# Performance work log

Measured on AMD Instinct MI355X. Metric: run time of the kernel, lower is better.

Reference implementation:

```python
import jax, jax.numpy as jnp
import numpy as np
from jax import lax


def _conv1x1(x, w, b=None):
    # x: [N,C,H,W], w: [O,C]
    y = jnp.einsum('nchw,oc->nohw', x, w)
    if b is not None:
        y = y + b[None, :, None, None]
    return y


def _bn(x, g, b, rm, rv):
    # eval-mode BatchNorm2d, eps=1e-5 (torch default)
    inv = g / jnp.sqrt(rv + 1e-5)
    return x * inv[None, :, None, None] + (b - rm * inv)[None, :, None, None]


def setup_inputs() -> dict:
    key = jax.random.key(0)
    ks = jax.random.split(key, 32)
    N, C1, C2, H, W = 16, 256, 256, 64, 64
    mid = C2 // 16  # local_att reduction=16
    f32 = jnp.float32
    def nrm(k, shp, s=0.05):
        return s * jax.random.normal(k, shp, f32)
    return dict(
        x1=jax.random.normal(ks[0], (N, C1, H, W), f32),
        x2=jax.random.normal(ks[1], (N, C2, H, W), f32),
        conv1_w=nrm(ks[2], (C2, C1)), conv1_b=nrm(ks[3], (C2,)),
        conv2_w=nrm(ks[4], (C2, C2)), conv2_b=nrm(ks[5], (C2,)),
        conv3_w=nrm(ks[6], (C2, C2)), conv3_b=nrm(ks[7], (C2,)),
        conv4_w=nrm(ks[8], (C2, C2)), conv4_b=nrm(ks[9], (C2,)),
        conv4g_w=nrm(ks[10], (1, C2)), conv4g_b=nrm(ks[11], (1,)),
        bn_g=1.0 + nrm(ks[12], (C2,)), bn_b=nrm(ks[13], (C2,)),
        bn_rm=nrm(ks[14], (C2,)), bn_rv=1.0 + 0.1 * jax.random.uniform(ks[15], (C2,), f32),
        gamma=jax.random.normal(ks[16], (C2, 1, 1), f32), beta=jnp.zeros((C2, 1, 1), f32),
        gate_w=nrm(ks[17], (C2, C2)), gate_b=nrm(ks[18], (C2,)),
        dw_w=nrm(ks[19], (C2, 1, 3, 3)), dw_b=nrm(ks[20], (C2,)),
        interact_w=nrm(ks[21], (C2 // 4, C2 // 4)), interact_b=0.5 + nrm(ks[22], (C2 // 4,)),
        ca_w=nrm(ks[23], (1, 1, 5)),  # channel_att conv1d kernel, k=5 for C=256
        la1_w=nrm(ks[24], (mid, C2)),
        la_bn_g=1.0 + nrm(ks[25], (mid,)), la_bn_b=nrm(ks[26], (mid,)),
        la_bn_rm=nrm(ks[27], (mid,)), la_bn_rv=1.0 + 0.1 * jax.random.uniform(ks[28], (mid,), f32),
        fh_w=nrm(ks[29], (C2, mid)), fw_w=nrm(ks[30], (C2, mid)),
    )


def reference(x1, x2, conv1_w, conv1_b, conv2_w, conv2_b, conv3_w, conv3_b,
              conv4_w, conv4_b, conv4g_w, conv4g_b, bn_g, bn_b, bn_rm, bn_rv,
              gamma, beta, gate_w, gate_b, dw_w, dw_b, interact_w, interact_b,
              ca_w, la1_w, la_bn_g, la_bn_b, la_bn_rm, la_bn_rv, fh_w, fw_w):
    N, _, H, W = x1.shape
    C = conv1_w.shape[0]
    g1 = _conv1x1(x1, conv1_w, conv1_b)
    w1 = jax.nn.sigmoid(_bn(g1, bn_g, bn_b, bn_rm, bn_rv))
    g2 = _conv1x1(x2, conv2_w, conv2_b)
    w2 = jax.nn.sigmoid(_bn(g2, bn_g, bn_b, bn_rm, bn_rv))
    XG = g1 + g2

    # channel_att: GAP -> conv1d(k=5) across channels -> sigmoid gate
    y = XG.mean((2, 3))[:, None, :]  # [N,1,C]
    y = lax.conv_general_dilated(y, ca_w, (1,), [(2, 2)],
                                 dimension_numbers=('NCH', 'OIH', 'NCH'))
    temp = XG * jax.nn.sigmoid(y[:, 0, :])[:, :, None, None]

    # spatial sigmoid gate then 4-way group interact + softmax reweight
    Xs = jax.nn.sigmoid(_conv1x1(XG, conv4g_w, conv4g_b)) * XG
    C4 = C // 4
    Xr = Xs.reshape(N, 4, C4, H, W)
    o1 = jnp.einsum('ngchw,oc->ngohw', Xr, interact_w) + interact_b[None, None, :, None, None]
    xmap = o1.reshape(N, 4, 1, C4 * H * W)
    xav = xmap / xmap.mean(-1, keepdims=True)
    soft = jax.nn.softmax(xav, axis=2)  # softmax over size-1 dim -> ones (faithful)
    out = (soft.reshape(N, 4, C4, H, W) * Xr).reshape(N, C, H, W)

    # per-group (16) normalization using X_GOBAL stats (std unbiased, ddof=1)
    GN = 16
    xs = XG.reshape(N, GN, -1)
    mu = xs.mean(-1, keepdims=True)
    sd = jnp.std(xs, axis=-1, keepdims=True, ddof=1)
    x_gui = ((out.reshape(N, GN, -1) - mu) / (sd + 1e-10)).reshape(N, C, H, W)
    x_gui = x_gui * gamma[None] + beta[None]

    # threshold masks vs global-avg sigmoid reweights
    rw = jax.nn.sigmoid(XG.mean((2, 3), keepdims=True))  # [N,C,1,1]
    up1 = rw >= w1
    up2 = rw >= w2
    zero = jnp.zeros((), XG.dtype)
    x_up = jnp.where(up1, XG, zero) + jnp.where(up2, XG, zero)
    x_low = jnp.where(~up1, XG, zero) + jnp.where(~up2, XG, zero)

    # low branch: dwconv3x3 -> 1x1 -> channel-softmax gate
    dw = lax.conv_general_dilated(x_low, dw_w, (1, 1), [(1, 1), (1, 1)],
                                  dimension_numbers=('NCHW', 'OIHW', 'NCHW'),
                                  feature_group_count=C) + dw_b[None, :, None, None]
    x11 = _conv1x1(dw, conv3_w, conv3_b)
    gate = jax.nn.softmax(jax.nn.relu(x_low.mean((2, 3)) @ gate_w.T + gate_b), axis=1)
    xL = x11 * gate[:, :, None, None] + _conv1x1(x_up, conv4_w, conv4_b) + x_gui + temp

    # local_att (coordinate attention)
    xh = jnp.swapaxes(xL.mean(3, keepdims=True), 2, 3)  # [N,C,1,H]
    xw = xL.mean(2, keepdims=True)                       # [N,C,1,W]
    yc = jax.nn.relu(_bn(_conv1x1(jnp.concatenate([xh, xw], 3), la1_w),
                         la_bn_g, la_bn_b, la_bn_rm, la_bn_rv))
    sh = jax.nn.sigmoid(_conv1x1(jnp.swapaxes(yc[..., :H], 2, 3), fh_w))  # [N,C,H,1]
    sw = jax.nn.sigmoid(_conv1x1(yc[..., H:], fw_w))                      # [N,C,1,W]
    return xL * sh * sw
```

## Files before the change

kernel.cpp:

```cpp
#include <hip/hip_runtime.h>
#include <cstddef>
#include <cstdint>

constexpr int NN = 16, CC = 256, HH = 64, WW = 64, HW = 64 * 64;
constexpr size_t FSZ = (size_t)NN * CC * HW;

typedef short bf16x8 __attribute__((ext_vector_type(8)));
typedef float f32x4 __attribute__((ext_vector_type(4)));

__device__ __forceinline__ float sigmoidf_(float x) { return 1.f / (1.f + expf(-x)); }

__device__ __forceinline__ unsigned short bf16_rne(float f) {
    uint32_t u = __builtin_bit_cast(uint32_t, f);
    u += 0x7FFFu + ((u >> 16) & 1u);
    return (unsigned short)(u >> 16);
}
__device__ __forceinline__ float bf16_tof(unsigned short h) {
    uint32_t u = ((uint32_t)h) << 16;
    return __builtin_bit_cast(float, u);
}


__global__ __launch_bounds__(256) void wsplit_kernel(
    const float* __restrict__ w1, const float* __restrict__ w2,
    const float* __restrict__ w3, const float* __restrict__ w4,
    unsigned short* __restrict__ w1h, unsigned short* __restrict__ w1m, unsigned short* __restrict__ w1l,
    unsigned short* __restrict__ w2h, unsigned short* __restrict__ w2m, unsigned short* __restrict__ w2l,
    unsigned short* __restrict__ w4h, unsigned short* __restrict__ w4l,
    unsigned short* __restrict__ w3b,
    float* __restrict__ zstat, float* __restrict__ zspix) {
    const int i = blockIdx.x * 256 + threadIdx.x;
    const int o = i >> 8, c = i & 255;
    const size_t fo = ((size_t)((o >> 4) * 8 + (c >> 5))) * 512 +
                      (size_t)(((c & 31) >> 3) * 128 + (o & 15) * 8 + (c & 7));
    {
        float x = w1[i];
        unsigned short h = bf16_rne(x); float r = x - bf16_tof(h);
        unsigned short m = bf16_rne(r); float r2 = r - bf16_tof(m);
        w1h[fo] = h; w1m[fo] = m; w1l[fo] = bf16_rne(r2);
    }
    {
        float x = w2[i];
        unsigned short h = bf16_rne(x); float r = x - bf16_tof(h);
        unsigned short m = bf16_rne(r); float r2 = r - bf16_tof(m);
        w2h[fo] = h; w2m[fo] = m; w2l[fo] = bf16_rne(r2);
    }
    {
        float x = w4[i];
        unsigned short h = bf16_rne(x); float r = x - bf16_tof(h);
        w4h[fo] = h; w4l[fo] = bf16_rne(r);
    }
    w3b[fo] = bf16_rne(w3[i]);
    if (i < 8192) zstat[i] = 0.f;
    zspix[i] = 0.f;
}

template <int NS>
__global__ __launch_bounds__(256) void tsplit_kernel(const float* __restrict__ X,
                                                     unsigned short* __restrict__ O0,
                                                     unsigned short* __restrict__ O1,
                                                     unsigned short* __restrict__ O2) {
    const int hw0 = blockIdx.x * 64, c0 = blockIdx.y * 64, n = blockIdx.z;
    __shared__ float sT[64][65];
    const int tid = threadIdx.x;
    {
        const int hwl = (tid & 15) << 2;
        const int cl = tid >> 4;
#pragma unroll
        for (int p = 0; p < 4; ++p) {
            const int c = cl + p * 16;
            const float4 v = *(const float4*)(X + ((size_t)(n * CC + c0 + c)) * HW + hw0 + hwl);
            sT[c][hwl] = v.x; sT[c][hwl + 1] = v.y; sT[c][hwl + 2] = v.z; sT[c][hwl + 3] = v.w;
        }
    }
    __syncthreads();
    const int hwl = tid >> 2, cb = (tid & 3) << 4;
    unsigned short h[16], m[16], l[16];
#pragma unroll
    for (int j = 0; j < 16; ++j) {
        const float x = sT[cb + j][hwl];
        const unsigned short hh = bf16_rne(x);
        h[j] = hh;
        if (NS >= 2) {
            const float r = x - bf16_tof(hh);
            const unsigned short mm = bf16_rne(r);
            m[j] = mm;
            if (NS >= 3) l[j] = bf16_rne(r - bf16_tof(mm));
        }
    }
    const size_t ob = ((size_t)(n * HW + hw0 + hwl)) * 256 + c0 + cb;
    *(int4*)(O0 + ob) = *(int4*)&h[0]; *(int4*)(O0 + ob + 8) = *(int4*)&h[8];
    if (NS >= 2) { *(int4*)(O1 + ob) = *(int4*)&m[0]; *(int4*)(O1 + ob + 8) = *(int4*)&m[8]; }
    if (NS >= 3) { *(int4*)(O2 + ob) = *(int4*)&l[0]; *(int4*)(O2 + ob + 8) = *(int4*)&l[8]; }
}

template <int NS>
__device__ __forceinline__ void mfma_core4(const unsigned short* __restrict__ X0,
                                           const unsigned short* __restrict__ X1,
                                           const unsigned short* __restrict__ X2,
                                           const unsigned short* __restrict__ W0,
                                           const unsigned short* __restrict__ W1,
                                           const unsigned short* __restrict__ W2,
                                           int n, int hw0, int o0, f32x4 (&acc)[2][4]) {
    __shared__ unsigned short sX[2][NS][64][40];
    const int tid = threadIdx.x;
    const int lane = tid & 63, wv = tid >> 6, quad = lane >> 4, nlo = lane & 15;
    const int srow = tid >> 2, skoff = (tid & 3) << 3;
    const unsigned short* Xs[3] = {X0, X1, X2};
    const unsigned short* Ws[3] = {W0, W1, W2};
    const size_t xg = ((size_t)(n * HW + hw0 + srow)) * 256 + skoff;
    const unsigned short* wp[NS];
#pragma unroll
    for (int s = 0; s < NS; ++s)
        wp[s] = Ws[s] + ((size_t)((o0 >> 4) + wv) * 8) * 512 + (size_t)lane * 8;

#pragma unroll
    for (int s = 0; s < NS; ++s)
        *(int4*)&sX[0][s][srow][skoff] = *(const int4*)(Xs[s] + xg);
    __syncthreads();

    for (int ks = 0; ks < 8; ++ks) {
        const int cur = ks & 1;
        int4 nx[NS];
        if (ks < 7) {
#pragma unroll
            for (int s = 0; s < NS; ++s) nx[s] = *(const int4*)(Xs[s] + xg + (ks + 1) * 32);
        }
        bf16x8 af[NS][2];
#pragma unroll
        for (int s = 0; s < NS; ++s)
#pragma unroll
            for (int f = 0; f < 2; ++f)
                af[s][f] = *(const bf16x8*)(wp[s] + ((size_t)(f * 32 + ks)) * 512);
#pragma unroll
        for (int nt = 0; nt < 4; ++nt) {
            bf16x8 bfr[NS];
#pragma unroll
            for (int s = 0; s < NS; ++s) bfr[s] = *(const bf16x8*)&sX[cur][s][nt * 16 + nlo][quad * 8];
#pragma unroll
            for (int f = 0; f < 2; ++f) {
                if (NS == 3) {
                    acc[f][nt] = __builtin_amdgcn_mfma_f32_16x16x32_bf16(af[1][f], bfr[1], acc[f][nt], 0, 0, 0);
                    acc[f][nt] = __builtin_amdgcn_mfma_f32_16x16x32_bf16(af[0][f], bfr[2], acc[f][nt], 0, 0, 0);
                    acc[f][nt] = __builtin_amdgcn_mfma_f32_16x16x32_bf16(af[2][f], bfr[0], acc[f][nt], 0, 0, 0);
                    acc[f][nt] = __builtin_amdgcn_mfma_f32_16x16x32_bf16(af[0][f], bfr[1], acc[f][nt], 0, 0, 0);
                    acc[f][nt] = __builtin_amdgcn_mfma_f32_16x16x32_bf16(af[1][f], bfr[0], acc[f][nt], 0, 0, 0);
                    acc[f][nt] = __builtin_amdgcn_mfma_f32_16x16x32_bf16(af[0][f], bfr[0], acc[f][nt], 0, 0, 0);
                } else if (NS == 2) {
                    acc[f][nt] = __builtin_amdgcn_mfma_f32_16x16x32_bf16(af[0][f], bfr[1], acc[f][nt], 0, 0, 0);
                    acc[f][nt] = __builtin_amdgcn_mfma_f32_16x16x32_bf16(af[1][f], bfr[0], acc[f][nt], 0, 0, 0);
                    acc[f][nt] = __builtin_amdgcn_mfma_f32_16x16x32_bf16(af[0][f], bfr[0], acc[f][nt], 0, 0, 0);
                } else {
                    acc[f][nt] = __builtin_amdgcn_mfma_f32_16x16x32_bf16(af[0][f], bfr[0], acc[f][nt], 0, 0, 0);
                }
            }
        }
        if (ks < 7) {
#pragma unroll
            for (int s = 0; s < NS; ++s) *(int4*)&sX[cur ^ 1][s][srow][skoff] = nx[s];
        }
        __syncthreads();
    }
}

__device__ __forceinline__ void mfma_core_pair(const unsigned short* __restrict__ XUH,
                                               const unsigned short* __restrict__ XUL,
                                               const unsigned short* __restrict__ XDW,
                                               const unsigned short* __restrict__ W4H,
                                               const unsigned short* __restrict__ W4L,
                                               const unsigned short* __restrict__ W3B,
                                               int n, int hw0, int o0,
                                               f32x4 (&acc_a)[2][4], f32x4 (&acc_b)[2][4]) {
    __shared__ unsigned short sX[2][3][64][40];
    const int tid = threadIdx.x;
    const int lane = tid & 63, wv = tid >> 6, quad = lane >> 4, nlo = lane & 15;
    const int srow = tid >> 2, skoff = (tid & 3) << 3;
    const unsigned short* Xs[3] = {XUH, XUL, XDW};
    const unsigned short* Ws[3] = {W4H, W4L, W3B};
    const size_t xg = ((size_t)(n * HW + hw0 + srow)) * 256 + skoff;
    const unsigned short* wp[3];
#pragma unroll
    for (int s = 0; s < 3; ++s)
        wp[s] = Ws[s] + ((size_t)((o0 >> 4) + wv) * 8) * 512 + (size_t)lane * 8;

#pragma unroll
    for (int s = 0; s < 3; ++s)
        *(int4*)&sX[0][s][srow][skoff] = *(const int4*)(Xs[s] + xg);
    __syncthreads();

    for (int ks = 0; ks < 8; ++ks) {
        const int cur = ks & 1;
        int4 nx[3];
        if (ks < 7) {
#pragma unroll
            for (int s = 0; s < 3; ++s) nx[s] = *(const int4*)(Xs[s] + xg + (ks + 1) * 32);
        }
        bf16x8 af[3][2];
#pragma unroll
        for (int s = 0; s < 3; ++s)
#pragma unroll
            for (int f = 0; f < 2; ++f)
                af[s][f] = *(const bf16x8*)(wp[s] + ((size_t)(f * 32 + ks)) * 512);
#pragma unroll
        for (int nt = 0; nt < 4; ++nt) {
            bf16x8 bfr[3];
#pragma unroll
            for (int s = 0; s < 3; ++s) bfr[s] = *(const bf16x8*)&sX[cur][s][nt * 16 + nlo][quad * 8];
#pragma unroll
            for (int f = 0; f < 2; ++f) {
                acc_a[f][nt] = __builtin_amdgcn_mfma_f32_16x16x32_bf16(af[0][f], bfr[1], acc_a[f][nt], 0, 0, 0);
                acc_a[f][nt] = __builtin_amdgcn_mfma_f32_16x16x32_bf16(af[1][f], bfr[0], acc_a[f][nt], 0, 0, 0);
                acc_a[f][nt] = __builtin_amdgcn_mfma_f32_16x16x32_bf16(af[0][f], bfr[0], acc_a[f][nt], 0, 0, 0);
                acc_b[f][nt] = __builtin_amdgcn_mfma_f32_16x16x32_bf16(af[2][f], bfr[2], acc_b[f][nt], 0, 0, 0);
            }
        }
        if (ks < 7) {
#pragma unroll
            for (int s = 0; s < 3; ++s) *(int4*)&sX[cur ^ 1][s][srow][skoff] = nx[s];
        }
        __syncthreads();
    }
}

template <int NS>
__global__ __launch_bounds__(256, 3) void gemm_mfma_kernel(
    const unsigned short* __restrict__ X0, const unsigned short* __restrict__ X1,
    const unsigned short* __restrict__ X2, const unsigned short* __restrict__ W0,
    const unsigned short* __restrict__ W1, const unsigned short* __restrict__ W2,
    const float* __restrict__ bias, float* __restrict__ Y) {
    const int hw0 = blockIdx.x * 64, o0 = blockIdx.y * 128, n = blockIdx.z;
    f32x4 acc[2][4] = {};
    mfma_core4<NS>(X0, X1, X2, W0, W1, W2, n, hw0, o0, acc);
    const int lane = threadIdx.x & 63, wv = threadIdx.x >> 6;
    const int quad = lane >> 4, nlo = lane & 15;
#pragma unroll
    for (int f = 0; f < 2; ++f) {
        const int om = o0 + f * 64 + wv * 16 + quad * 4;
#pragma unroll
        for (int nt = 0; nt < 4; ++nt) {
            const int hw = hw0 + nt * 16 + nlo;
#pragma unroll
            for (int r = 0; r < 4; ++r) {
                const int o = om + r;
                Y[((size_t)(n * CC + o)) * HW + hw] = acc[f][nt][r] + bias[o];
            }
        }
    }
}

__global__ __launch_bounds__(256, 3) void gemm_xg_kernel(
    const unsigned short* __restrict__ X0, const unsigned short* __restrict__ X1,
    const unsigned short* __restrict__ X2, const unsigned short* __restrict__ W0,
    const unsigned short* __restrict__ W1, const unsigned short* __restrict__ W2,
    const float* __restrict__ bias, const float* __restrict__ g1,
    const float* __restrict__ cgw,
    float* __restrict__ XG, float* __restrict__ sum_c, float* __restrict__ sq_c,
    float* __restrict__ s_pix) {
    const int hw0 = blockIdx.x * 64, o0 = blockIdx.y * 128, n = blockIdx.z;
    f32x4 acc[2][4] = {};
    mfma_core4<3>(X0, X1, X2, W0, W1, W2, n, hw0, o0, acc);
    __shared__ float sRed[4][64];
    const int lane = threadIdx.x & 63, wv = threadIdx.x >> 6;
    const int quad = lane >> 4, nlo = lane & 15;
    float pnt[4] = {0.f, 0.f, 0.f, 0.f};
#pragma unroll
    for (int f = 0; f < 2; ++f) {
        const int om = o0 + f * 64 + wv * 16 + quad * 4;
#pragma unroll
        for (int r = 0; r < 4; ++r) {
            const int o = om + r;
            const float b = bias[o];
            const float wg = cgw[o];
            float s = 0.f, q = 0.f;
#pragma unroll
            for (int nt = 0; nt < 4; ++nt) {
                const int hw = hw0 + nt * 16 + nlo;
                const size_t rowi = ((size_t)(n * CC + o)) * HW + hw;
                const float xgv = acc[f][nt][r] + b + g1[rowi];
                XG[rowi] = xgv;
                s += xgv; q += xgv * xgv;
                pnt[nt] += wg * xgv;
            }
#pragma unroll
            for (int off = 1; off < 16; off <<= 1) { s += __shfl_xor(s, off); q += __shfl_xor(q, off); }
            if (nlo == 0) { atomicAdd(&sum_c[n * CC + o], s); atomicAdd(&sq_c[n * CC + o], q); }
        }
    }
#pragma unroll
    for (int nt = 0; nt < 4; ++nt) {
        float p = pnt[nt];
        p += __shfl_xor(p, 16); p += __shfl_xor(p, 32);
        if (quad == 0) sRed[wv][nt * 16 + nlo] = p;
    }
    __syncthreads();
    if (threadIdx.x < 64) {
        const float s2 = sRed[0][threadIdx.x] + sRed[1][threadIdx.x] +
                         sRed[2][threadIdx.x] + sRed[3][threadIdx.x];
        atomicAdd(&s_pix[n * HW + hw0 + threadIdx.x], s2);
    }
}

__global__ __launch_bounds__(256, 3) void gemm_final_kernel(
    const unsigned short* __restrict__ XUH, const unsigned short* __restrict__ XUL,
    const unsigned short* __restrict__ XDW,
    const unsigned short* __restrict__ W4H, const unsigned short* __restrict__ W4L,
    const unsigned short* __restrict__ W3B,
    const float* __restrict__ b3, const float* __restrict__ b4,
    const float* __restrict__ XG, const float* __restrict__ s_pix,
    const float* __restrict__ cgb,
    const float* __restrict__ gate, const float* __restrict__ ca_sig,
    const float* __restrict__ mu_g, const float* __restrict__ isd_g,
    const float* __restrict__ gamma, const float* __restrict__ beta,
    float* __restrict__ out) {
    const int hw0 = blockIdx.x * 64, o0 = blockIdx.y * 128, n = blockIdx.z;
    f32x4 acc_a[2][4] = {};
    f32x4 acc_b[2][4] = {};
    mfma_core_pair(XUH, XUL, XDW, W4H, W4L, W3B, n, hw0, o0, acc_a, acc_b);
    const int lane = threadIdx.x & 63, wv = threadIdx.x >> 6;
    const int quad = lane >> 4, nlo = lane & 15;
    const float cgb0 = cgb[0];
#pragma unroll
    for (int f = 0; f < 2; ++f) {
        const int om = o0 + f * 64 + wv * 16 + quad * 4;
#pragma unroll
        for (int nt = 0; nt < 4; ++nt) {
            const int hw = hw0 + nt * 16 + nlo;
            const int pix = n * HW + hw;
            const float sp = sigmoidf_(s_pix[pix] + cgb0);
#pragma unroll
            for (int r = 0; r < 4; ++r) {
                const int o = om + r;
                const float g = gate[n * CC + o];
                const float cs = ca_sig[n * CC + o];
                const float mu = mu_g[n * 16 + (o >> 4)];
                const float isd = isd_g[n * 16 + (o >> 4)];
                const size_t rowi = ((size_t)(n * CC + o)) * HW + hw;
                const float xg = XG[rowi];
                const float gui = (sp * xg - mu) * isd * gamma[o] + beta[o];
                out[rowi] = (acc_b[f][nt][r] + b3[o]) * g + (acc_a[f][nt][r] + b4[o]) + gui + xg * cs;
            }
        }
    }
}

__global__ __launch_bounds__(256) void stats2_kernel(const float* __restrict__ sum_c,
                                                     const float* __restrict__ sq_c,
                                                     const float* __restrict__ caw,
                                                     float* __restrict__ rw,
                                                     float* __restrict__ ca_sig,
                                                     float* __restrict__ mu_g,
                                                     float* __restrict__ isd_g,
                                                     float* __restrict__ xlow_sum) {
    const int n = blockIdx.x, c = threadIdx.x;
    __shared__ float m[256];
    const float mean = sum_c[n * CC + c] * (1.f / (float)HW);
    m[c] = mean;
    rw[n * CC + c] = sigmoidf_(mean);
    xlow_sum[n * CC + c] = 0.f;
    __syncthreads();
    float y = 0.f;
#pragma unroll
    for (int k = 0; k < 5; ++k) {
        const int cc = c - 2 + k;
        if (cc >= 0 && cc < 256) y += m[cc] * caw[k];
    }
    ca_sig[n * CC + c] = sigmoidf_(y);
    if (c < 16) {
        float S = 0.f, Q = 0.f;
        for (int j = 0; j < 16; ++j) {
            S += sum_c[n * CC + c * 16 + j];
            Q += sq_c[n * CC + c * 16 + j];
        }
        const float cnt = 65536.f;
        const float mu = S / cnt;
        float var = (Q - S * S / cnt) * (1.f / (cnt - 1.f));
        var = fmaxf(var, 0.f);
        mu_g[n * 16 + c] = mu;
        isd_g[n * 16 + c] = 1.f / (sqrtf(var) + 1e-10f);
    }
}

__global__ __launch_bounds__(256) void masks_split_kernel(
    float* g1_xlow,
    const float* __restrict__ XG,
    const float* __restrict__ rw,
    const float* __restrict__ bng, const float* __restrict__ bnb,
    const float* __restrict__ bnrm, const float* __restrict__ bnrv,
    unsigned short* __restrict__ O0, unsigned short* __restrict__ O1,
    float* __restrict__ xlow_sum) {
    const int hw0 = blockIdx.x * 64, c0 = blockIdx.y * 64, n = blockIdx.z;
    __shared__ float sT[64][65];
    const int tid = threadIdx.x;
    const int cl = tid >> 2;
    const int q = tid & 3;
    const int c = c0 + cl;
    const float inv = bng[c] / sqrtf(bnrv[c] + 1e-5f);
    const float off = bnb[c] - bnrm[c] * inv;
    const float rwv = rw[n * CC + c];
    const size_t rowb = ((size_t)(n * CC + c)) * HW + hw0;
    float lsum = 0.f;
#pragma unroll
    for (int j = 0; j < 4; ++j) {
        const int hwl = q * 4 + j * 16;
        const float4 a = *(const float4*)(g1_xlow + rowb + hwl);
        const float4 x = *(const float4*)(XG + rowb + hwl);
        const float* ap = &a.x; const float* xp = &x.x;
        float4 xlv;
        float* xlp = &xlv.x;
#pragma unroll
        for (int e = 0; e < 4; ++e) {
            const float g2e = xp[e] - ap[e];
            const float w1 = sigmoidf_(inv * ap[e] + off);
            const float w2 = sigmoidf_(inv * g2e + off);
            const float cu = (rwv >= w1 ? 1.f : 0.f) + (rwv >= w2 ? 1.f : 0.f);
            const float xu = xp[e] * cu;
            const float xl = xp[e] * (2.f - cu);
            sT[cl][hwl + e] = xu;
            xlp[e] = xl;
            lsum += xl;
        }
        *(float4*)(g1_xlow + rowb + hwl) = xlv;
    }
    lsum += __shfl_xor(lsum, 1);
    lsum += __shfl_xor(lsum, 2);
    if (q == 0) atomicAdd(&xlow_sum[n * CC + c], lsum);
    __syncthreads();
    const int hwl2 = tid >> 2, cb = (tid & 3) << 4;
    unsigned short h[16], m[16];
#pragma unroll
    for (int j = 0; j < 16; ++j) {
        const float x = sT[cb + j][hwl2];
        const unsigned short hh = bf16_rne(x);
        h[j] = hh;
        m[j] = bf16_rne(x - bf16_tof(hh));
    }
    const size_t ob = ((size_t)(n * HW + hw0 + hwl2)) * 256 + c0 + cb;
    *(int4*)(O0 + ob) = *(int4*)&h[0]; *(int4*)(O0 + ob + 8) = *(int4*)&h[8];
    *(int4*)(O1 + ob) = *(int4*)&m[0]; *(int4*)(O1 + ob + 8) = *(int4*)&m[8];
}

__global__ __launch_bounds__(256) void gate_kernel(const float* __restrict__ xlow_sum,
                                                   const float* __restrict__ gatew,
                                                   const float* __restrict__ gateb,
                                                   float* __restrict__ gate) {
    const int n = blockIdx.x, c = threadIdx.x;
    __shared__ float xm[256];
    __shared__ float red[256];
    xm[c] = xlow_sum[n * CC + c] * (1.f / (float)HW);
    __syncthreads();
    float acc = gateb[c];
    const float* wr = gatew + (size_t)c * 256;
#pragma unroll 8
    for (int k = 0; k < 256; ++k) acc += xm[k] * wr[k];
    const float v = fmaxf(acc, 0.f);
    red[c] = v;
    __syncthreads();
    for (int s = 128; s > 0; s >>= 1) {
        if (c < s) red[c] = fmaxf(red[c], red[c + s]);
        __syncthreads();
    }
    const float mx = red[0];
    __syncthreads();
    const float e = expf(v - mx);
    red[c] = e;
    __syncthreads();
    for (int s = 128; s > 0; s >>= 1) {
        if (c < s) red[c] += red[c + s];
        __syncthreads();
    }
    gate[n * CC + c] = e / red[0];
}

__global__ __launch_bounds__(256) void dwconv_kernel(const float* __restrict__ xlow,
                                                     const float* __restrict__ dww,
                                                     const float* __restrict__ dwb,
                                                     float* __restrict__ out) {
    const int c = blockIdx.x & 255;
    __shared__ float sl[64][65];
    const size_t base = (size_t)blockIdx.x * HW;
    for (int r = 0; r < 16; ++r) {
        const int idx = threadIdx.x + r * 256;
        sl[idx >> 6][idx & 63] = xlow[base + idx];
    }
    float wk[9];
#pragma unroll
    for (int j = 0; j < 9; ++j) wk[j] = dww[c * 9 + j];
    const float bias = dwb[c];
    __syncthreads();
    for (int r = 0; r < 16; ++r) {
        const int idx = threadIdx.x + r * 256;
        const int h = idx >> 6, w = idx & 63;
        float acc = bias;
#pragma unroll
        for (int dh = 0; dh < 3; ++dh) {
            const int hh = h + dh - 1;
            if (hh < 0 || hh > 63) continue;
#pragma unroll
            for (int dw2 = 0; dw2 < 3; ++dw2) {
                const int ww2 = w + dw2 - 1;
                if (ww2 < 0 || ww2 > 63) continue;
                acc += sl[hh][ww2] * wk[dh * 3 + dw2];
            }
        }
        out[base + idx] = acc;
    }
}

__global__ __launch_bounds__(256) void pool_kernel(const float* __restrict__ xL,
                                                   float* __restrict__ xh,
                                                   float* __restrict__ xw) {
    __shared__ float sl[64][65];
    const size_t base = (size_t)blockIdx.x * HW;
    for (int r = 0; r < 16; ++r) {
        const int idx = threadIdx.x + r * 256;
        sl[idx >> 6][idx & 63] = xL[base + idx];
    }
    __syncthreads();
    const int t = threadIdx.x;
    if (t < 64) {
        float s = 0.f;
        for (int w = 0; w < 64; ++w) s += sl[t][w];
        xh[(size_t)blockIdx.x * 64 + t] = s * (1.f / 64.f);
    } else if (t < 128) {
        const int w = t - 64;
        float s = 0.f;
        for (int h = 0; h < 64; ++h) s += sl[h][w];
        xw[(size_t)blockIdx.x * 64 + w] = s * (1.f / 64.f);
    }
}

__global__ __launch_bounds__(256) void local_att_kernel(const float* __restrict__ xh,
                                                        const float* __restrict__ xw,
                                                        const float* __restrict__ la1w,
                                                        const float* __restrict__ lag,
                                                        const float* __restrict__ lab,
                                                        const float* __restrict__ larm,
                                                        const float* __restrict__ larv,
                                                        const float* __restrict__ fhw,
                                                        const float* __restrict__ fww,
                                                        float* __restrict__ sh,
                                                        float* __restrict__ sw) {
    const int n = blockIdx.x;
    __shared__ float w1s[16 * 256];
    __shared__ float fhs[256 * 16];
    __shared__ float fws[256 * 16];
    __shared__ float ycs[16][128];
    for (int i = threadIdx.x; i < 4096; i += 256) {
        w1s[i] = la1w[i];
        fhs[i] = fhw[i];
        fws[i] = fww[i];
    }
    __syncthreads();
    for (int idx = threadIdx.x; idx < 2048; idx += 256) {
        const int m = idx >> 7, p = idx & 127;
        const float* vsrc = (p < 64) ? (xh + (size_t)n * CC * 64 + p)
                                     : (xw + (size_t)n * CC * 64 + (p - 64));
        float acc = 0.f;
#pragma unroll 8
        for (int c = 0; c < 256; ++c) acc += w1s[m * 256 + c] * vsrc[(size_t)c * 64];
        const float inv = lag[m] / sqrtf(larv[m] + 1e-5f);
        const float off = lab[m] - larm[m] * inv;
        ycs[m][p] = fmaxf(inv * acc + off, 0.f);
    }
    __syncthreads();
    for (int idx = threadIdx.x; idx < 16384; idx += 256) {
        const int c = idx >> 6, h = idx & 63;
        float a1 = 0.f, a2 = 0.f;
#pragma unroll
        for (int m = 0; m < 16; ++m) {
            a1 += fhs[c * 16 + m] * ycs[m][h];
            a2 += fws[c * 16 + m] * ycs[m][64 + h];
        }
        sh[(size_t)n * CC * 64 + idx] = sigmoidf_(a1);
        sw[(size_t)n * CC * 64 + idx] = sigmoidf_(a2);
    }
}

__global__ __launch_bounds__(256) void final_kernel(const float* __restrict__ xL,
                                                    const float* __restrict__ sh,
                                                    const float* __restrict__ sw,
                                                    float* __restrict__ out) {
    __shared__ float shs[64], sws[64];
    const int t = threadIdx.x;
    if (t < 64) shs[t] = sh[(size_t)blockIdx.x * 64 + t];
    else if (t < 128) sws[t - 64] = sw[(size_t)blockIdx.x * 64 + (t - 64)];
    __syncthreads();
    const size_t base = (size_t)blockIdx.x * HW;
#pragma unroll 4
    for (int r = 0; r < 16; ++r) {
        const int idx = t + r * 256;
        out[base + idx] = xL[base + idx] * shs[idx >> 6] * sws[idx & 63];
    }
}

extern "C" void kernel_launch(void* const* d_in, const int* in_sizes, int n_in,
                              void* d_out, int out_size, void* d_ws, size_t ws_size,
                              hipStream_t stream) {
    const float* x1 = (const float*)d_in[0];
    const float* x2 = (const float*)d_in[1];
    const float* c1w = (const float*)d_in[2];
    const float* c1b = (const float*)d_in[3];
    const float* c2w = (const float*)d_in[4];
    const float* c2b = (const float*)d_in[5];
    const float* c3w = (const float*)d_in[6];
    const float* c3b = (const float*)d_in[7];
    const float* c4w = (const float*)d_in[8];
    const float* c4b = (const float*)d_in[9];
    const float* cgw = (const float*)d_in[10];
    const float* cgb = (const float*)d_in[11];
    const float* bng = (const float*)d_in[12];
    const float* bnb = (const float*)d_in[13];
    const float* bnrm = (const float*)d_in[14];
    const float* bnrv = (const float*)d_in[15];
    const float* gamma = (const float*)d_in[16];
    const float* beta = (const float*)d_in[17];
    const float* gatew = (const float*)d_in[18];
    const float* gateb = (const float*)d_in[19];
    const float* dww = (const float*)d_in[20];
    const float* dwb = (const float*)d_in[21];
    const float* caw = (const float*)d_in[24];
    const float* la1w = (const float*)d_in[25];
    const float* lag = (const float*)d_in[26];
    const float* lab = (const float*)d_in[27];
    const float* larm = (const float*)d_in[28];
    const float* larv = (const float*)d_in[29];
    const float* fhw = (const float*)d_in[30];
    const float* fww = (const float*)d_in[31];

    float* ws = (float*)d_ws;
    float* buf0 = ws;
    float* buf1 = ws + FSZ;
    float* buf2 = ws + 2 * FSZ;
    float* sp = ws + 3 * FSZ;
    float* sum_c = sp;    sp += 4096;
    float* sq_c = sp;     sp += 4096;
    float* rw = sp;       sp += 4096;
    float* ca_sig = sp;   sp += 4096;
    float* xlow_sum = sp; sp += 4096;
    float* mu_g = sp;     sp += 256;
    float* isd_g = sp;    sp += 256;
    float* s_pix = sp;    sp += (size_t)NN * HW;
    float* xh = sp;       sp += (size_t)NN * CC * 64;
    float* xwb = sp;      sp += (size_t)NN * CC * 64;
    float* shb = sp;      sp += (size_t)NN * CC * 64;
    float* swb = sp;      sp += (size_t)NN * CC * 64;
    unsigned short* wsp = (unsigned short*)shb;
    unsigned short* w1h = wsp + 0 * 65536;
    unsigned short* w1m = wsp + 1 * 65536;
    unsigned short* w1l = wsp + 2 * 65536;
    unsigned short* w2h = wsp + 3 * 65536;
    unsigned short* w2m = wsp + 4 * 65536;
    unsigned short* w2l = wsp + 5 * 65536;
    unsigned short* w4h = wsp + 6 * 65536;
    unsigned short* w4l = wsp + 7 * 65536;
    unsigned short* w3b = wsp + 8 * 65536;

    float* out = (float*)d_out;

    const dim3 gt(HW / 64, CC / 64, NN);
    const dim3 gg(HW / 64, CC / 128, NN);

    wsplit_kernel<<<256, 256, 0, stream>>>(c1w, c2w, c3w, c4w, w1h, w1m, w1l,
                                           w2h, w2m, w2l, w4h, w4l, w3b,
                                           sum_c, s_pix);
    {
        unsigned short* sx0 = (unsigned short*)buf1;
        unsigned short* sx1 = (unsigned short*)buf1 + FSZ;
        unsigned short* sx2 = (unsigned short*)buf2;
        tsplit_kernel<3><<<gt, 256, 0, stream>>>(x1, sx0, sx1, sx2);
        gemm_mfma_kernel<3><<<gg, 256, 0, stream>>>(sx0, sx1, sx2, w1h, w1m, w1l, c1b, buf0);
    }
    {
        unsigned short* sx0 = (unsigned short*)out;
        unsigned short* sx1 = (unsigned short*)out + FSZ;
        unsigned short* sx2 = (unsigned short*)buf2;
        tsplit_kernel<3><<<gt, 256, 0, stream>>>(x2, sx0, sx1, sx2);
        gemm_xg_kernel<<<gg, 256, 0, stream>>>(sx0, sx1, sx2, w2h, w2m, w2l, c2b,
                                               buf0, cgw, buf1, sum_c, sq_c, s_pix);
    }
    stats2_kernel<<<NN, 256, 0, stream>>>(sum_c, sq_c, caw, rw, ca_sig, mu_g, isd_g, xlow_sum);
    {
        unsigned short* ux0 = (unsigned short*)out;
        unsigned short* ux1 = (unsigned short*)out + FSZ;
        masks_split_kernel<<<gt, 256, 0, stream>>>(buf0, buf1, rw, bng, bnb, bnrm, bnrv,
                                                   ux0, ux1, xlow_sum);
    }
    float* gate = sum_c;
    gate_kernel<<<NN, 256, 0, stream>>>(xlow_sum, gatew, gateb, gate);
    dwconv_kernel<<<NN * CC, 256, 0, stream>>>(buf0, dww, dwb, buf0);
    {
        unsigned short* sx0 = (unsigned short*)buf2;
        tsplit_kernel<1><<<gt, 256, 0, stream>>>(buf0, sx0, nullptr, nullptr);
    }
    {
        unsigned short* ux0 = (unsigned short*)out;
        unsigned short* ux1 = (unsigned short*)out + FSZ;
        unsigned short* sx0 = (unsigned short*)buf2;
        gemm_final_kernel<<<gg, 256, 0, stream>>>(ux0, ux1, sx0, w4h, w4l, w3b,
                                                  c3b, c4b, buf1, s_pix, cgb,
                                                  gate, ca_sig, mu_g, isd_g, gamma, beta,
                                                  buf0);
    }
    pool_kernel<<<NN * CC, 256, 0, stream>>>(buf0, xh, xwb);
    local_att_kernel<<<NN, 256, 0, stream>>>(xh, xwb, la1w, lag, lab, larm, larv,
                                             fhw, fww, shb, swb);
    final_kernel<<<NN * CC, 256, 0, stream>>>(buf0, shb, swb, out);
}
```

Baseline: 669.4 us.

## Use full-channel tiles, direct global-to-LDS loads and swizzled LDS in MFMA GEMMs

The first two GEMMs now compute all 256 output channels per block instead of 128, so the X tile is loaded from global memory once rather than twice. Because each block now owns a full pixel column, the s_pix atomicAdd is replaced with a plain store. All GEMM cores stage X through global_load_lds into an XOR-swizzled 64-wide LDS tile with K steps of 64 and fewer barriers. The trade-off is more accumulator registers per thread and half as many blocks for the first two GEMMs, which can lower occupancy.

```diff
diff --git a/kernel.cpp b/kernel.cpp
--- a/kernel.cpp
+++ b/kernel.cpp
@@ -18,6 +18,11 @@
 __device__ __forceinline__ float bf16_tof(unsigned short h) {
     uint32_t u = ((uint32_t)h) << 16;
     return __builtin_bit_cast(float, u);
+}
+
+__device__ __forceinline__ void gload16(const void* g, void* l) {
+    __builtin_amdgcn_global_load_lds((const __attribute__((address_space(1))) void*)g,
+                                     (__attribute__((address_space(3))) void*)l, 16, 0, 0);
 }
 
 
@@ -94,148 +99,172 @@
     if (NS >= 3) { *(int4*)(O2 + ob) = *(int4*)&l[0]; *(int4*)(O2 + ob + 8) = *(int4*)&l[8]; }
 }
 
-template <int NS>
-__device__ __forceinline__ void mfma_core4(const unsigned short* __restrict__ X0,
+__device__ __forceinline__ void mfma_core7(const unsigned short* __restrict__ X0,
                                            const unsigned short* __restrict__ X1,
                                            const unsigned short* __restrict__ X2,
                                            const unsigned short* __restrict__ W0,
                                            const unsigned short* __restrict__ W1,
                                            const unsigned short* __restrict__ W2,
-                                           int n, int hw0, int o0, f32x4 (&acc)[2][4]) {
-    __shared__ unsigned short sX[2][NS][64][40];
+                                           int n, int hw0, f32x4 (&acc)[4][4]) {
+    __shared__ unsigned short sX[2][3][64][64];
     const int tid = threadIdx.x;
     const int lane = tid & 63, wv = tid >> 6, quad = lane >> 4, nlo = lane & 15;
-    const int srow = tid >> 2, skoff = (tid & 3) << 3;
+    const int srl = lane >> 3;
+    const int sch = (lane & 7) ^ srl;
     const unsigned short* Xs[3] = {X0, X1, X2};
     const unsigned short* Ws[3] = {W0, W1, W2};
-    const size_t xg = ((size_t)(n * HW + hw0 + srow)) * 256 + skoff;
-    const unsigned short* wp[NS];
-#pragma unroll
-    for (int s = 0; s < NS; ++s)
-        wp[s] = Ws[s] + ((size_t)((o0 >> 4) + wv) * 8) * 512 + (size_t)lane * 8;
-
-#pragma unroll
-    for (int s = 0; s < NS; ++s)
-        *(int4*)&sX[0][s][srow][skoff] = *(const int4*)(Xs[s] + xg);
-    __syncthreads();
-
-    for (int ks = 0; ks < 8; ++ks) {
-        const int cur = ks & 1;
-        int4 nx[NS];
-        if (ks < 7) {
-#pragma unroll
-            for (int s = 0; s < NS; ++s) nx[s] = *(const int4*)(Xs[s] + xg + (ks + 1) * 32);
-        }
-        bf16x8 af[NS][2];
-#pragma unroll
-        for (int s = 0; s < NS; ++s)
-#pragma unroll
-            for (int f = 0; f < 2; ++f)
-                af[s][f] = *(const bf16x8*)(wp[s] + ((size_t)(f * 32 + ks)) * 512);
+    const size_t xgb = ((size_t)(n * HW + hw0 + wv * 16 + srl)) * 256 + sch * 8;
+    const unsigned short* wp[3];
+#pragma unroll
+    for (int s = 0; s < 3; ++s)
+        wp[s] = Ws[s] + ((size_t)(wv * 4) * 8) * 512 + (size_t)lane * 8;
+
+    int roff[2][4];
+#pragma unroll
+    for (int s2 = 0; s2 < 2; ++s2)
 #pragma unroll
         for (int nt = 0; nt < 4; ++nt) {
-            bf16x8 bfr[NS];
-#pragma unroll
-            for (int s = 0; s < NS; ++s) bfr[s] = *(const bf16x8*)&sX[cur][s][nt * 16 + nlo][quad * 8];
-#pragma unroll
-            for (int f = 0; f < 2; ++f) {
-                if (NS == 3) {
+            const int rrow = nt * 16 + nlo;
+            roff[s2][nt] = rrow * 64 + ((s2 * 4 + quad) ^ (rrow & 7)) * 8;
+        }
+
+#pragma unroll
+    for (int s = 0; s < 3; ++s)
+#pragma unroll
+        for (int j = 0; j < 2; ++j)
+            gload16(Xs[s] + xgb + (size_t)j * 8 * 256, &sX[0][s][wv * 16 + j * 8][0]);
+    __syncthreads();
+
+#pragma unroll
+    for (int kt = 0; kt < 4; ++kt) {
+        const int cur = kt & 1;
+        if (kt < 3) {
+#pragma unroll
+            for (int s = 0; s < 3; ++s)
+#pragma unroll
+                for (int j = 0; j < 2; ++j)
+                    gload16(Xs[s] + xgb + (kt + 1) * 64 + (size_t)j * 8 * 256,
+                            &sX[cur ^ 1][s][wv * 16 + j * 8][0]);
+        }
+#pragma unroll
+        for (int s2 = 0; s2 < 2; ++s2) {
+            const int kk = kt * 2 + s2;
+            bf16x8 af[3][4];
+#pragma unroll
+            for (int s = 0; s < 3; ++s)
+#pragma unroll
+                for (int f = 0; f < 4; ++f)
+                    af[s][f] = *(const bf16x8*)(wp[s] + ((size_t)(f * 8 + kk)) * 512);
+#pragma unroll
+            for (int nt = 0; nt < 4; ++nt) {
+                bf16x8 bfr[3];
+#pragma unroll
+                for (int s = 0; s < 3; ++s)
+                    bfr[s] = *(const bf16x8*)&sX[cur][s][0][roff[s2][nt]];
+#pragma unroll
+                for (int f = 0; f < 4; ++f) {
                     acc[f][nt] = __builtin_amdgcn_mfma_f32_16x16x32_bf16(af[1][f], bfr[1], acc[f][nt], 0, 0, 0);
                     acc[f][nt] = __builtin_amdgcn_mfma_f32_16x16x32_bf16(af[0][f], bfr[2], acc[f][nt], 0, 0, 0);
                     acc[f][nt] = __builtin_amdgcn_mfma_f32_16x16x32_bf16(af[2][f], bfr[0], acc[f][nt], 0, 0, 0);
                     acc[f][nt] = __builtin_amdgcn_mfma_f32_16x16x32_bf16(af[0][f], bfr[1], acc[f][nt], 0, 0, 0);
                     acc[f][nt] = __builtin_amdgcn_mfma_f32_16x16x32_bf16(af[1][f], bfr[0], acc[f][nt], 0, 0, 0);
                     acc[f][nt] = __builtin_amdgcn_mfma_f32_16x16x32_bf16(af[0][f], bfr[0], acc[f][nt], 0, 0, 0);
-                } else if (NS == 2) {
-                    acc[f][nt] = __builtin_amdgcn_mfma_f32_16x16x32_bf16(af[0][f], bfr[1], acc[f][nt], 0, 0, 0);
-                    acc[f][nt] = __builtin_amdgcn_mfma_f32_16x16x32_bf16(af[1][f], bfr[0], acc[f][nt], 0, 0, 0);
-                    acc[f][nt] = __builtin_amdgcn_mfma_f32_16x16x32_bf16(af[0][f], bfr[0], acc[f][nt], 0, 0, 0);
-                } else {
-                    acc[f][nt] = __builtin_amdgcn_mfma_f32_16x16x32_bf16(af[0][f], bfr[0], acc[f][nt], 0, 0, 0);
                 }
             }
         }
-        if (ks < 7) {
-#pragma unroll
-            for (int s = 0; s < NS; ++s) *(int4*)&sX[cur ^ 1][s][srow][skoff] = nx[s];
-        }
         __syncthreads();
     }
 }
 
-__device__ __forceinline__ void mfma_core_pair(const unsigned short* __restrict__ XUH,
-                                               const unsigned short* __restrict__ XUL,
-                                               const unsigned short* __restrict__ XDW,
-                                               const unsigned short* __restrict__ W4H,
-                                               const unsigned short* __restrict__ W4L,
-                                               const unsigned short* __restrict__ W3B,
-                                               int n, int hw0, int o0,
-                                               f32x4 (&acc_a)[2][4], f32x4 (&acc_b)[2][4]) {
-    __shared__ unsigned short sX[2][3][64][40];
+__device__ __forceinline__ void mfma_core_pair7(const unsigned short* __restrict__ XUH,
+                                                const unsigned short* __restrict__ XUL,
+                                                const unsigned short* __restrict__ XDW,
+                                                const unsigned short* __restrict__ W4H,
+                                                const unsigned short* __restrict__ W4L,
+                                                const unsigned short* __restrict__ W3B,
+                                                int n, int hw0, int o0,
+                                                f32x4 (&acc_a)[2][4], f32x4 (&acc_b)[2][4]) {
+    __shared__ unsigned short sX[2][3][64][64];
     const int tid = threadIdx.x;
     const int lane = tid & 63, wv = tid >> 6, quad = lane >> 4, nlo = lane & 15;
-    const int srow = tid >> 2, skoff = (tid & 3) << 3;
+    const int srl = lane >> 3;
+    const int sch = (lane & 7) ^ srl;
     const unsigned short* Xs[3] = {XUH, XUL, XDW};
     const unsigned short* Ws[3] = {W4H, W4L, W3B};
-    const size_t xg = ((size_t)(n * HW + hw0 + srow)) * 256 + skoff;
+    const size_t xgb = ((size_t)(n * HW + hw0 + wv * 16 + srl)) * 256 + sch * 8;
     const unsigned short* wp[3];
 #pragma unroll
     for (int s = 0; s < 3; ++s)
         wp[s] = Ws[s] + ((size_t)((o0 >> 4) + wv) * 8) * 512 + (size_t)lane * 8;
 
+    int roff[2][4];
+#pragma unroll
+    for (int s2 = 0; s2 < 2; ++s2)
+#pragma unroll
+        for (int nt = 0; nt < 4; ++nt) {
+            const int rrow = nt * 16 + nlo;
+            roff[s2][nt] = rrow * 64 + ((s2 * 4 + quad) ^ (rrow & 7)) * 8;
+        }
+
 #pragma unroll
     for (int s = 0; s < 3; ++s)
-        *(int4*)&sX[0][s][srow][skoff] = *(const int4*)(Xs[s] + xg);
-    __syncthreads();
-
-    for (int ks = 0; ks < 8; ++ks) {
-        const int cur = ks & 1;
-        int4 nx[3];
-        if (ks < 7) {
-#pragma unroll
-            for (int s = 0; s < 3; ++s) nx[s] = *(const int4*)(Xs[s] + xg + (ks + 1) * 32);
-        }
-        bf16x8 af[3][2];
-#pragma unroll
-        for (int s = 0; s < 3; ++s)
-#pragma unroll
-            for (int f = 0; f < 2; ++f)
-                af[s][f] = *(const bf16x8*)(wp[s] + ((size_t)(f * 32 + ks)) * 512);
-#pragma unroll
-        for (int nt = 0; nt < 4; ++nt) {
-            bf16x8 bfr[3];
-#pragma unroll
-            for (int s = 0; s < 3; ++s) bfr[s] = *(const bf16x8*)&sX[cur][s][nt * 16 + nlo][quad * 8];
-#pragma unroll
-            for (int f = 0; f < 2; ++f) {
-                acc_a[f][nt] = __builtin_amdgcn_mfma_f32_16x16x32_bf16(af[0][f], bfr[1], acc_a[f][nt], 0, 0, 0);
-                acc_a[f][nt] = __builtin_amdgcn_mfma_f32_16x16x32_bf16(af[1][f], bfr[0], acc_a[f][nt], 0, 0, 0);
-                acc_a[f][nt] = __builtin_amdgcn_mfma_f32_16x16x32_bf16(af[0][f], bfr[0], acc_a[f][nt], 0, 0, 0);
-                acc_b[f][nt] = __builtin_amdgcn_mfma_f32_16x16x32_bf16(af[2][f], bfr[2], acc_b[f][nt], 0, 0, 0);
+#pragma unroll
+        for (int j = 0; j < 2; ++j)
+            gload16(Xs[s] + xgb + (size_t)j * 8 * 256, &sX[0][s][wv * 16 + j * 8][0]);
+    __syncthreads();
+
+#pragma unroll
+    for (int kt = 0; kt < 4; ++kt) {
+        const int cur = kt & 1;
+        if (kt < 3) {
+#pragma unroll
+            for (int s = 0; s < 3; ++s)
+#pragma unroll
+                for (int j = 0; j < 2; ++j)
+                    gload16(Xs[s] + xgb + (kt + 1) * 64 + (size_t)j * 8 * 256,
+                            &sX[cur ^ 1][s][wv * 16 + j * 8][0]);
+        }
+#pragma unroll
+        for (int s2 = 0; s2 < 2; ++s2) {
+            const int kk = kt * 2 + s2;
+            bf16x8 af[3][2];
+#pragma unroll
+            for (int s = 0; s < 3; ++s)
+#pragma unroll
+                for (int f = 0; f < 2; ++f)
+                    af[s][f] = *(const bf16x8*)(wp[s] + ((size_t)(f * 32 + kk)) * 512);
+#pragma unroll
+            for (int nt = 0; nt < 4; ++nt) {
+                bf16x8 bfr[3];
+#pragma unroll
+                for (int s = 0; s < 3; ++s)
+                    bfr[s] = *(const bf16x8*)&sX[cur][s][0][roff[s2][nt]];
+#pragma unroll
+                for (int f = 0; f < 2; ++f) {
+                    acc_a[f][nt] = __builtin_amdgcn_mfma_f32_16x16x32_bf16(af[0][f], bfr[1], acc_a[f][nt], 0, 0, 0);
+                    acc_a[f][nt] = __builtin_amdgcn_mfma_f32_16x16x32_bf16(af[1][f], bfr[0], acc_a[f][nt], 0, 0, 0);
+                    acc_a[f][nt] = __builtin_amdgcn_mfma_f32_16x16x32_bf16(af[0][f], bfr[0], acc_a[f][nt], 0, 0, 0);
+                    acc_b[f][nt] = __builtin_amdgcn_mfma_f32_16x16x32_bf16(af[2][f], bfr[2], acc_b[f][nt], 0, 0, 0);
+                }
             }
         }
-        if (ks < 7) {
-#pragma unroll
-            for (int s = 0; s < 3; ++s) *(int4*)&sX[cur ^ 1][s][srow][skoff] = nx[s];
-        }
         __syncthreads();
     }
 }
 
-template <int NS>
 __global__ __launch_bounds__(256, 3) void gemm_mfma_kernel(
     const unsigned short* __restrict__ X0, const unsigned short* __restrict__ X1,
     const unsigned short* __restrict__ X2, const unsigned short* __restrict__ W0,
     const unsigned short* __restrict__ W1, const unsigned short* __restrict__ W2,
     const float* __restrict__ bias, float* __restrict__ Y) {
-    const int hw0 = blockIdx.x * 64, o0 = blockIdx.y * 128, n = blockIdx.z;
-    f32x4 acc[2][4] = {};
-    mfma_core4<NS>(X0, X1, X2, W0, W1, W2, n, hw0, o0, acc);
+    const int hw0 = blockIdx.x * 64, n = blockIdx.z;
+    f32x4 acc[4][4] = {};
+    mfma_core7(X0, X1, X2, W0, W1, W2, n, hw0, acc);
     const int lane = threadIdx.x & 63, wv = threadIdx.x >> 6;
     const int quad = lane >> 4, nlo = lane & 15;
 #pragma unroll
-    for (int f = 0; f < 2; ++f) {
-        const int om = o0 + f * 64 + wv * 16 + quad * 4;
+    for (int f = 0; f < 4; ++f) {
+        const int om = wv * 64 + f * 16 + quad * 4;
 #pragma unroll
         for (int nt = 0; nt < 4; ++nt) {
             const int hw = hw0 + nt * 16 + nlo;
@@ -256,16 +285,16 @@
     const float* __restrict__ cgw,
     float* __restrict__ XG, float* __restrict__ sum_c, float* __restrict__ sq_c,
     float* __restrict__ s_pix) {
-    const int hw0 = blockIdx.x * 64, o0 = blockIdx.y * 128, n = blockIdx.z;
-    f32x4 acc[2][4] = {};
-    mfma_core4<3>(X0, X1, X2, W0, W1, W2, n, hw0, o0, acc);
+    const int hw0 = blockIdx.x * 64, n = blockIdx.z;
+    f32x4 acc[4][4] = {};
+    mfma_core7(X0, X1, X2, W0, W1, W2, n, hw0, acc);
     __shared__ float sRed[4][64];
     const int lane = threadIdx.x & 63, wv = threadIdx.x >> 6;
     const int quad = lane >> 4, nlo = lane & 15;
     float pnt[4] = {0.f, 0.f, 0.f, 0.f};
 #pragma unroll
-    for (int f = 0; f < 2; ++f) {
-        const int om = o0 + f * 64 + wv * 16 + quad * 4;
+    for (int f = 0; f < 4; ++f) {
+        const int om = wv * 64 + f * 16 + quad * 4;
 #pragma unroll
         for (int r = 0; r < 4; ++r) {
             const int o = om + r;
@@ -294,9 +323,8 @@
     }
     __syncthreads();
     if (threadIdx.x < 64) {
-        const float s2 = sRed[0][threadIdx.x] + sRed[1][threadIdx.x] +
-                         sRed[2][threadIdx.x] + sRed[3][threadIdx.x];
-        atomicAdd(&s_pix[n * HW + hw0 + threadIdx.x], s2);
+        s_pix[n * HW + hw0 + threadIdx.x] = sRed[0][threadIdx.x] + sRed[1][threadIdx.x] +
+                                            sRed[2][threadIdx.x] + sRed[3][threadIdx.x];
     }
 }
 
@@ -315,7 +343,7 @@
     const int hw0 = blockIdx.x * 64, o0 = blockIdx.y * 128, n = blockIdx.z;
     f32x4 acc_a[2][4] = {};
     f32x4 acc_b[2][4] = {};
-    mfma_core_pair(XUH, XUL, XDW, W4H, W4L, W3B, n, hw0, o0, acc_a, acc_b);
+    mfma_core_pair7(XUH, XUL, XDW, W4H, W4L, W3B, n, hw0, o0, acc_a, acc_b);
     const int lane = threadIdx.x & 63, wv = threadIdx.x >> 6;
     const int quad = lane >> 4, nlo = lane & 15;
     const float cgb0 = cgb[0];
@@ -658,7 +686,8 @@
     float* out = (float*)d_out;
 
     const dim3 gt(HW / 64, CC / 64, NN);
-    const dim3 gg(HW / 64, CC / 128, NN);
+    const dim3 g1g(HW / 64, 1, NN);
+    const dim3 g2g(HW / 64, CC / 128, NN);
 
     wsplit_kernel<<<256, 256, 0, stream>>>(c1w, c2w, c3w, c4w, w1h, w1m, w1l,
                                            w2h, w2m, w2l, w4h, w4l, w3b,
@@ -668,15 +697,15 @@
         unsigned short* sx1 = (unsigned short*)buf1 + FSZ;
         unsigned short* sx2 = (unsigned short*)buf2;
         tsplit_kernel<3><<<gt, 256, 0, stream>>>(x1, sx0, sx1, sx2);
-        gemm_mfma_kernel<3><<<gg, 256, 0, stream>>>(sx0, sx1, sx2, w1h, w1m, w1l, c1b, buf0);
+        gemm_mfma_kernel<<<g1g, 256, 0, stream>>>(sx0, sx1, sx2, w1h, w1m, w1l, c1b, buf0);
     }
     {
         unsigned short* sx0 = (unsigned short*)out;
         unsigned short* sx1 = (unsigned short*)out + FSZ;
         unsigned short* sx2 = (unsigned short*)buf2;
         tsplit_kernel<3><<<gt, 256, 0, stream>>>(x2, sx0, sx1, sx2);
-        gemm_xg_kernel<<<gg, 256, 0, stream>>>(sx0, sx1, sx2, w2h, w2m, w2l, c2b,
-                                               buf0, cgw, buf1, sum_c, sq_c, s_pix);
+        gemm_xg_kernel<<<g1g, 256, 0, stream>>>(sx0, sx1, sx2, w2h, w2m, w2l, c2b,
+                                                buf0, cgw, buf1, sum_c, sq_c, s_pix);
     }
     stats2_kernel<<<NN, 256, 0, stream>>>(sum_c, sq_c, caw, rw, ca_sig, mu_g, isd_g, xlow_sum);
     {
@@ -696,10 +725,10 @@
         unsigned short* ux0 = (unsigned short*)out;
         unsigned short* ux1 = (unsigned short*)out + FSZ;
         unsigned short* sx0 = (unsigned short*)buf2;
-        gemm_final_kernel<<<gg, 256, 0, stream>>>(ux0, ux1, sx0, w4h, w4l, w3b,
-                                                  c3b, c4b, buf1, s_pix, cgb,
-                                                  gate, ca_sig, mu_g, isd_g, gamma, beta,
-                                                  buf0);
+        gemm_final_kernel<<<g2g, 256, 0, stream>>>(ux0, ux1, sx0, w4h, w4l, w3b,
+                                                   c3b, c4b, buf1, s_pix, cgb,
+                                                   gate, ca_sig, mu_g, isd_g, gamma, beta,
+                                                   buf0);
     }
     pool_kernel<<<NN * CC, 256, 0, stream>>>(buf0, xh, xwb);
     local_att_kernel<<<NN, 256, 0, stream>>>(xh, xwb, la1w, lag, lab, larm, larv,
```

Measured after the change: 687.4 us. +2.7%, slower.
